# Kernel optimization log

Hardware: AMD Instinct MI355X
Metric: run time of the kernel (lower is better)

## Reference

```python
import jax, jax.numpy as jnp
import numpy as np

N, H, V = 2048, 2048, 32000

def setup_inputs() -> dict:
    key = jax.random.key(0)
    k1, k2, k3 = jax.random.split(key, 3)
    x = jax.random.normal(k1, (N, H), dtype=jnp.float32)
    y = jax.random.normal(k2, (N, V), dtype=jnp.float32)
    # nn.Linear default init: U(-1/sqrt(H), 1/sqrt(H))
    bound = 1.0 / np.sqrt(H)
    W = jax.random.uniform(k3, (V, H), dtype=jnp.float32, minval=-bound, maxval=bound)
    return {"x": x, "y": y, "W": W}

def reference(x, y, W):
    # logits = x @ W^T : [N, V]
    logits = jnp.einsum('nh,vh->nv', x, W)
    # MSE with 'mean' reduction over all elements
    diff = logits - y
    return jnp.mean(diff * diff)
```

## Files before the change

### kernel.cpp

```cpp
#include <hip/hip_runtime.h>

#define MDIM 2048
#define KDIM 2048
#define VDIM 32000
#define TILE 128
#define BK 64
#define LDAB (2 * KDIM)

typedef __bf16 bf16x8 __attribute__((ext_vector_type(8)));
typedef float f32x4 __attribute__((ext_vector_type(4)));
typedef unsigned short ushort_t;

__device__ __forceinline__ unsigned short f32_to_bf16_rne(float f) {
    unsigned u = __float_as_uint(f);
    u += 0x7FFFu + ((u >> 16) & 1u);
    return (unsigned short)(u >> 16);
}

__global__ __launch_bounds__(256) void cast_inplace_rows4_kernel(
        float* __restrict__ rows, float* zero_out) {
    if (zero_out && blockIdx.x == 0 && threadIdx.x == 0) *zero_out = 0.0f;
    float* base = rows + (long)blockIdx.x * 4 * KDIM;
    const int t = threadIdx.x;
    float4 v[8];
#pragma unroll
    for (int rr = 0; rr < 4; ++rr) {
        const float4* p = reinterpret_cast<const float4*>(base + rr * KDIM + t * 8);
        v[2 * rr]     = p[0];
        v[2 * rr + 1] = p[1];
    }
    __syncthreads();
#pragma unroll
    for (int rr = 0; rr < 4; ++rr) {
        union { unsigned short h[8]; uint4 u; } r;
        float4 a = v[2 * rr], b = v[2 * rr + 1];
        r.h[0] = f32_to_bf16_rne(a.x);
        r.h[1] = f32_to_bf16_rne(a.y);
        r.h[2] = f32_to_bf16_rne(a.z);
        r.h[3] = f32_to_bf16_rne(a.w);
        r.h[4] = f32_to_bf16_rne(b.x);
        r.h[5] = f32_to_bf16_rne(b.y);
        r.h[6] = f32_to_bf16_rne(b.z);
        r.h[7] = f32_to_bf16_rne(b.w);
        reinterpret_cast<uint4*>(base + rr * KDIM)[t] = r.u;
    }
}

__global__ __launch_bounds__(256) void gemm_mse_kernel(
        const unsigned short* __restrict__ A,
        const unsigned short* __restrict__ B,
        const float* __restrict__ Y,
        float* __restrict__ out) {
    __shared__ __align__(16) unsigned short As[TILE * BK];
    __shared__ __align__(16) unsigned short Bs[TILE * BK];

    const int tid  = threadIdx.x;
    const int lane = tid & 63;
    const int wave = tid >> 6;
    const int wr = (wave >> 1) * 64;
    const int wc = (wave & 1) * 64;
    const int m0 = lane & 15;
    const int q  = lane >> 4;

    const long rowBase = (long)blockIdx.x * TILE;
    const long colBase = (long)blockIdx.y * TILE;

    f32x4 acc[4][4];
#pragma unroll
    for (int i = 0; i < 4; ++i)
#pragma unroll
        for (int j = 0; j < 4; ++j)
            acc[i][j] = (f32x4){0.f, 0.f, 0.f, 0.f};

    const unsigned short* agp[4];
    const unsigned short* bgp[4];
    unsigned short* asp[4];
    unsigned short* bsp[4];
#pragma unroll
    for (int s = 0; s < 4; ++s) {
        int l = tid + 256 * s;
        int row = l >> 3;
        int segg = (l & 7) ^ (row & 7);
        agp[s] = A + (rowBase + row) * LDAB + segg * 8;
        bgp[s] = B + (colBase + row) * LDAB + segg * 8;
        asp[s] = As + l * 8;
        bsp[s] = Bs + l * 8;
    }

    const int sxor = m0 & 7;
    const unsigned short* aRow = As + (wr + m0) * BK;
    const unsigned short* bRow = Bs + (wc + m0) * BK;
    const int off0 = ((q)     ^ sxor) * 8;
    const int off1 = ((4 + q) ^ sxor) * 8;

    for (int kt = 0; kt < KDIM; kt += BK) {
        __syncthreads();
#pragma unroll
        for (int s = 0; s < 4; ++s) {
            __builtin_amdgcn_global_load_lds(
                (const __attribute__((address_space(1))) void*)(agp[s] + kt),
                (__attribute__((address_space(3))) void*)asp[s], 16, 0, 0);
            __builtin_amdgcn_global_load_lds(
                (const __attribute__((address_space(1))) void*)(bgp[s] + kt),
                (__attribute__((address_space(3))) void*)bsp[s], 16, 0, 0);
        }
        __syncthreads();

#pragma unroll
        for (int h = 0; h < 2; ++h) {
            const int off = h ? off1 : off0;
            bf16x8 af[4], bfr[4];
#pragma unroll
            for (int i = 0; i < 4; ++i)
                af[i] = *(const bf16x8*)(const void*)(aRow + i * 16 * BK + off);
#pragma unroll
            for (int j = 0; j < 4; ++j)
                bfr[j] = *(const bf16x8*)(const void*)(bRow + j * 16 * BK + off);
#pragma unroll
            for (int i = 0; i < 4; ++i)
#pragma unroll
                for (int j = 0; j < 4; ++j)
                    acc[i][j] = __builtin_amdgcn_mfma_f32_16x16x32_bf16(
                        af[i], bfr[j], acc[i][j], 0, 0, 0);
        }
    }

    float sum = 0.f;
#pragma unroll
    for (int i = 0; i < 4; ++i) {
#pragma unroll
        for (int j = 0; j < 4; ++j) {
            long gr = rowBase + wr + i * 16 + q * 4;
            long gc = colBase + wc + j * 16 + m0;
            const float* yp = Y + gr * VDIM + gc;
#pragma unroll
            for (int r = 0; r < 4; ++r) {
                float d = acc[i][j][r] - yp[(long)r * VDIM];
                sum += d * d;
            }
        }
    }
    sum += __shfl_down(sum, 32);
    sum += __shfl_down(sum, 16);
    sum += __shfl_down(sum, 8);
    sum += __shfl_down(sum, 4);
    sum += __shfl_down(sum, 2);
    sum += __shfl_down(sum, 1);
    __syncthreads();
    float* red = (float*)(void*)As;
    if (lane == 0) red[wave] = sum;
    __syncthreads();
    if (tid == 0) {
        float t = (red[0] + red[1]) + (red[2] + red[3]);
        atomicAdd(out, t * (1.0f / ((float)MDIM * (float)VDIM)));
    }
}

extern "C" void kernel_launch(void* const* d_in, const int* in_sizes, int n_in,
                              void* d_out, int out_size, void* d_ws, size_t ws_size,
                              hipStream_t stream) {
    float* x = (float*)d_in[0];
    const float* y = (const float*)d_in[1];
    float* W = (float*)d_in[2];
    float* out = (float*)d_out;
    (void)d_ws; (void)ws_size;

    cast_inplace_rows4_kernel<<<MDIM / 4, 256, 0, stream>>>(x, out);
    cast_inplace_rows4_kernel<<<VDIM / 4, 256, 0, stream>>>(W, nullptr);

    dim3 grid(MDIM / TILE, VDIM / TILE);
    gemm_mse_kernel<<<grid, 256, 0, stream>>>(
        (const unsigned short*)x, (const unsigned short*)W, y, out);
}
```

Before: 814.7 us.

## Use 256x256 tiles with double-buffered 8-phase pipelined MFMA GEMM and tile swizzle

Grows the block tile to 256x256 with 512 threads and 8 waves per block. The main loop becomes a hand-scheduled 8-phase pipeline over double-buffered LDS: asynchronous global-to-LDS loads for the next K slices are issued between MFMA groups, with explicit vmcnt and lgkmcnt waits, barriers and raised wave priority. It also remaps block indices with a swizzle so that consecutive blocks share W tiles in cache. The aim is to hide global load latency and raise arithmetic intensity, at the cost of more registers and LDS per block and a fragile manual wait-count schedule.

```diff
diff --git a/kernel.cpp b/kernel.cpp
--- a/kernel.cpp
+++ b/kernel.cpp
@@ -3,13 +3,13 @@
 #define MDIM 2048
 #define KDIM 2048
 #define VDIM 32000
-#define TILE 128
+#define BM 256
+#define BN 256
 #define BK 64
 #define LDAB (2 * KDIM)
 
 typedef __bf16 bf16x8 __attribute__((ext_vector_type(8)));
 typedef float f32x4 __attribute__((ext_vector_type(4)));
-typedef unsigned short ushort_t;
 
 __device__ __forceinline__ unsigned short f32_to_bf16_rne(float f) {
     unsigned u = __float_as_uint(f);
@@ -46,96 +46,159 @@
     }
 }
 
-__global__ __launch_bounds__(256) void gemm_mse_kernel(
+
+#define BMFMA(a, b, c) __builtin_amdgcn_mfma_f32_16x16x32_bf16(a, b, c, 0, 0, 0)
+
+#define GLL16(gp, lp) __builtin_amdgcn_global_load_lds( \
+    (const __attribute__((address_space(1))) void*)(gp), \
+    (__attribute__((address_space(3))) void*)(lp), 16, 0, 0)
+
+#define STAGE_A(bi, hf, kt) do { \
+    GLL16(aG0 + (size_t)(hf) * 128 * LDAB + (kt), &As[bi][(hf) * 128 * BK + dOff0]); \
+    GLL16(aG1 + (size_t)(hf) * 128 * LDAB + (kt), &As[bi][(hf) * 128 * BK + dOff1]); \
+} while (0)
+
+#define STAGE_B(bi, hf, kt) do { \
+    GLL16(bG0 + (size_t)(hf) * 128 * LDAB + (kt), &Bs[bi][(hf) * 128 * BK + dOff0]); \
+    GLL16(bG1 + (size_t)(hf) * 128 * LDAB + (kt), &Bs[bi][(hf) * 128 * BK + dOff1]); \
+} while (0)
+
+#define DS_B1(bi, n) do { \
+    const unsigned short* br_ = &Bs[bi][(wcol + (n) * 16 + m0) * BK]; \
+    bfr[2 * (n)]     = *(const bf16x8*)(const void*)(br_ + off0); \
+    bfr[2 * (n) + 1] = *(const bf16x8*)(const void*)(br_ + off1); \
+} while (0)
+#define DS_B8(bi) do { DS_B1(bi, 0); DS_B1(bi, 1); DS_B1(bi, 2); DS_B1(bi, 3); } while (0)
+
+#define DS_A2(bi, mb) do { \
+    const unsigned short* ar_ = &As[bi][(wrow + (mb) * 16 + m0) * BK]; \
+    af[0] = *(const bf16x8*)(const void*)(ar_ + off0); \
+    af[1] = *(const bf16x8*)(const void*)(ar_ + off1); \
+    af[2] = *(const bf16x8*)(const void*)(ar_ + 16 * BK + off0); \
+    af[3] = *(const bf16x8*)(const void*)(ar_ + 16 * BK + off1); \
+} while (0)
+
+#define MFMA16(mb) do { \
+    acc[(mb)][0]     = BMFMA(af[0], bfr[0], acc[(mb)][0]); \
+    acc[(mb) + 1][0] = BMFMA(af[2], bfr[0], acc[(mb) + 1][0]); \
+    acc[(mb)][1]     = BMFMA(af[0], bfr[2], acc[(mb)][1]); \
+    acc[(mb) + 1][1] = BMFMA(af[2], bfr[2], acc[(mb) + 1][1]); \
+    acc[(mb)][2]     = BMFMA(af[0], bfr[4], acc[(mb)][2]); \
+    acc[(mb) + 1][2] = BMFMA(af[2], bfr[4], acc[(mb) + 1][2]); \
+    acc[(mb)][3]     = BMFMA(af[0], bfr[6], acc[(mb)][3]); \
+    acc[(mb) + 1][3] = BMFMA(af[2], bfr[6], acc[(mb) + 1][3]); \
+    acc[(mb)][0]     = BMFMA(af[1], bfr[1], acc[(mb)][0]); \
+    acc[(mb) + 1][0] = BMFMA(af[3], bfr[1], acc[(mb) + 1][0]); \
+    acc[(mb)][1]     = BMFMA(af[1], bfr[3], acc[(mb)][1]); \
+    acc[(mb) + 1][1] = BMFMA(af[3], bfr[3], acc[(mb) + 1][1]); \
+    acc[(mb)][2]     = BMFMA(af[1], bfr[5], acc[(mb)][2]); \
+    acc[(mb) + 1][2] = BMFMA(af[3], bfr[5], acc[(mb) + 1][2]); \
+    acc[(mb)][3]     = BMFMA(af[1], bfr[7], acc[(mb)][3]); \
+    acc[(mb) + 1][3] = BMFMA(af[3], bfr[7], acc[(mb) + 1][3]); \
+} while (0)
+
+#define BAR() do { __builtin_amdgcn_s_barrier(); __builtin_amdgcn_sched_barrier(0); } while (0)
+#define WAITKL() do { asm volatile("s_waitcnt lgkmcnt(0)" ::: "memory"); \
+                      __builtin_amdgcn_sched_barrier(0); } while (0)
+#define VMCNT4() do { asm volatile("s_waitcnt vmcnt(4)" ::: "memory"); \
+                      __builtin_amdgcn_sched_barrier(0); } while (0)
+#define VMCNT0() do { asm volatile("s_waitcnt vmcnt(0)" ::: "memory"); \
+                      __builtin_amdgcn_sched_barrier(0); } while (0)
+
+#define PHASE(dsr, stg, wt, bi, mb) do { \
+    dsr; stg; wt; \
+    BAR(); WAITKL(); \
+    __builtin_amdgcn_s_setprio(1); \
+    MFMA16(mb); \
+    __builtin_amdgcn_s_setprio(0); \
+    BAR(); \
+} while (0)
+
+__global__ __launch_bounds__(512, 2) void gemm_mse_kernel(
         const unsigned short* __restrict__ A,
         const unsigned short* __restrict__ B,
         const float* __restrict__ Y,
         float* __restrict__ out) {
-    __shared__ __align__(16) unsigned short As[TILE * BK];
-    __shared__ __align__(16) unsigned short Bs[TILE * BK];
+    __shared__ __align__(16) unsigned short As[2][BM * BK];
+    __shared__ __align__(16) unsigned short Bs[2][BN * BK];
 
     const int tid  = threadIdx.x;
     const int lane = tid & 63;
-    const int wave = tid >> 6;
-    const int wr = (wave >> 1) * 64;
-    const int wc = (wave & 1) * 64;
+    const int wid  = tid >> 6;
+    const int wrow = (wid >> 2) * 128;
+    const int wcol = (wid & 3) * 64;
     const int m0 = lane & 15;
     const int q  = lane >> 4;
 
-    const long rowBase = (long)blockIdx.x * TILE;
-    const long colBase = (long)blockIdx.y * TILE;
-
-    f32x4 acc[4][4];
-#pragma unroll
-    for (int i = 0; i < 4; ++i)
+    const int lin = blockIdx.x;
+    const int swz = (lin & 7) * 125 + (lin >> 3);
+    const int tm = swz & 7;
+    const int tv = swz >> 3;
+    const long rowBase = (long)tm * BM;
+    const long colBase = (long)tv * BN;
+
+    f32x4 acc[8][4];
+#pragma unroll
+    for (int i = 0; i < 8; ++i)
 #pragma unroll
         for (int j = 0; j < 4; ++j)
             acc[i][j] = (f32x4){0.f, 0.f, 0.f, 0.f};
 
-    const unsigned short* agp[4];
-    const unsigned short* bgp[4];
-    unsigned short* asp[4];
-    unsigned short* bsp[4];
-#pragma unroll
-    for (int s = 0; s < 4; ++s) {
-        int l = tid + 256 * s;
-        int row = l >> 3;
-        int segg = (l & 7) ^ (row & 7);
-        agp[s] = A + (rowBase + row) * LDAB + segg * 8;
-        bgp[s] = B + (colBase + row) * LDAB + segg * 8;
-        asp[s] = As + l * 8;
-        bsp[s] = Bs + l * 8;
-    }
+    const int l0 = tid, l1 = tid + 512;
+    const int r0 = l0 >> 3, r1 = l1 >> 3;
+    const int g0 = (l0 & 7) ^ (r0 & 7), g1 = (l1 & 7) ^ (r1 & 7);
+    const unsigned short* aG0 = A + (size_t)(rowBase + r0) * LDAB + g0 * 8;
+    const unsigned short* aG1 = A + (size_t)(rowBase + r1) * LDAB + g1 * 8;
+    const unsigned short* bG0 = B + (size_t)(colBase + r0) * LDAB + g0 * 8;
+    const unsigned short* bG1 = B + (size_t)(colBase + r1) * LDAB + g1 * 8;
+    const int dOff0 = l0 * 8, dOff1 = l1 * 8;
 
     const int sxor = m0 & 7;
-    const unsigned short* aRow = As + (wr + m0) * BK;
-    const unsigned short* bRow = Bs + (wc + m0) * BK;
-    const int off0 = ((q)     ^ sxor) * 8;
+    const int off0 = ((0 + q) ^ sxor) * 8;
     const int off1 = ((4 + q) ^ sxor) * 8;
 
-    for (int kt = 0; kt < KDIM; kt += BK) {
-        __syncthreads();
-#pragma unroll
-        for (int s = 0; s < 4; ++s) {
-            __builtin_amdgcn_global_load_lds(
-                (const __attribute__((address_space(1))) void*)(agp[s] + kt),
-                (__attribute__((address_space(3))) void*)asp[s], 16, 0, 0);
-            __builtin_amdgcn_global_load_lds(
-                (const __attribute__((address_space(1))) void*)(bgp[s] + kt),
-                (__attribute__((address_space(3))) void*)bsp[s], 16, 0, 0);
-        }
-        __syncthreads();
-
-#pragma unroll
-        for (int h = 0; h < 2; ++h) {
-            const int off = h ? off1 : off0;
-            bf16x8 af[4], bfr[4];
-#pragma unroll
-            for (int i = 0; i < 4; ++i)
-                af[i] = *(const bf16x8*)(const void*)(aRow + i * 16 * BK + off);
-#pragma unroll
-            for (int j = 0; j < 4; ++j)
-                bfr[j] = *(const bf16x8*)(const void*)(bRow + j * 16 * BK + off);
-#pragma unroll
-            for (int i = 0; i < 4; ++i)
-#pragma unroll
-                for (int j = 0; j < 4; ++j)
-                    acc[i][j] = __builtin_amdgcn_mfma_f32_16x16x32_bf16(
-                        af[i], bfr[j], acc[i][j], 0, 0, 0);
-        }
-    }
+    bf16x8 af[4];
+    bf16x8 bfr[8];
+
+    STAGE_A(0, 0, 0); STAGE_A(0, 1, 0);
+    STAGE_B(0, 0, 0); STAGE_B(0, 1, 0);
+    STAGE_B(1, 0, BK); STAGE_B(1, 1, BK);
+    VMCNT4();
+    BAR();
+
+    for (int i = 0; i < 16; ++i) {
+        const int ktb  = i * 2 * BK;
+        const int ktA1 = ktb + BK;
+        int ktN  = ktb + 2 * BK;
+        if (ktN  > KDIM - BK) ktN  = KDIM - BK;
+        int ktN1 = ktb + 3 * BK;
+        if (ktN1 > KDIM - BK) ktN1 = KDIM - BK;
+
+        PHASE({ DS_B8(0); DS_A2(0, 0); },
+              { STAGE_A(1, 0, ktA1); STAGE_A(1, 1, ktA1); }, , 0, 0);
+        PHASE(DS_A2(0, 2), STAGE_B(0, 0, ktN), , 0, 2);
+        PHASE(DS_A2(0, 4), STAGE_B(0, 1, ktN), , 0, 4);
+        PHASE(DS_A2(0, 6), , VMCNT4(), 0, 6);
+        PHASE({ DS_B8(1); DS_A2(1, 0); }, STAGE_A(0, 0, ktN), , 1, 0);
+        PHASE(DS_A2(1, 2), STAGE_A(0, 1, ktN), , 1, 2);
+        PHASE(DS_A2(1, 4), STAGE_B(1, 0, ktN1), , 1, 4);
+        PHASE(DS_A2(1, 6), STAGE_B(1, 1, ktN1), VMCNT4(), 1, 6);
+    }
+
+    VMCNT0();
+    BAR();
 
     float sum = 0.f;
 #pragma unroll
-    for (int i = 0; i < 4; ++i) {
-#pragma unroll
-        for (int j = 0; j < 4; ++j) {
-            long gr = rowBase + wr + i * 16 + q * 4;
-            long gc = colBase + wc + j * 16 + m0;
-            const float* yp = Y + gr * VDIM + gc;
+    for (int m = 0; m < 8; ++m) {
+#pragma unroll
+        for (int n = 0; n < 4; ++n) {
+            long gr = rowBase + wrow + m * 16 + q * 4;
+            long gc = colBase + wcol + n * 16 + m0;
+            const float* yp = Y + gr * (long)VDIM + gc;
 #pragma unroll
             for (int r = 0; r < 4; ++r) {
-                float d = acc[i][j][r] - yp[(long)r * VDIM];
+                float d = acc[m][n][r] - yp[(long)r * VDIM];
                 sum += d * d;
             }
         }
@@ -146,12 +209,13 @@
     sum += __shfl_down(sum, 4);
     sum += __shfl_down(sum, 2);
     sum += __shfl_down(sum, 1);
-    __syncthreads();
     float* red = (float*)(void*)As;
-    if (lane == 0) red[wave] = sum;
+    if (lane == 0) red[wid] = sum;
     __syncthreads();
     if (tid == 0) {
-        float t = (red[0] + red[1]) + (red[2] + red[3]);
+        float t = 0.f;
+#pragma unroll
+        for (int w = 0; w < 8; ++w) t += red[w];
         atomicAdd(out, t * (1.0f / ((float)MDIM * (float)VDIM)));
     }
 }
@@ -168,7 +232,7 @@
     cast_inplace_rows4_kernel<<<MDIM / 4, 256, 0, stream>>>(x, out);
     cast_inplace_rows4_kernel<<<VDIM / 4, 256, 0, stream>>>(W, nullptr);
 
-    dim3 grid(MDIM / TILE, VDIM / TILE);
-    gemm_mse_kernel<<<grid, 256, 0, stream>>>(
+    dim3 grid((MDIM / BM) * (VDIM / BN));
+    gemm_mse_kernel<<<grid, 512, 0, stream>>>(
         (const unsigned short*)x, (const unsigned short*)W, y, out);
 }
```

New measurement: 740.2 us. 9.1% less time.

## Use 256x256 tiles with double-buffered LDS, 32x32 MFMA, and swizzled grid

Applied to the files above, without the earlier changes.

The GEMM+MSE kernel moves from 128x128 tiles to 256x256 tiles with 32x32x16 bf16 MFMA. It double-buffers LDS so global-to-LDS loads for the next K tile overlap compute, and it interleaves LDS fragment reads with MFMA groups using explicit waitcnt and setprio. A 1D grid with swizzled tile ordering is meant to improve L2 reuse, and Y is now read with float4 loads. The bigger tile raises arithmetic intensity but uses 128 KB of LDS and many registers, which forces one block per CU. The grid shrinks to 1000 blocks over 256 CUs, leaving some tail imbalance.

```diff
diff --git a/kernel.cpp b/kernel.cpp
--- a/kernel.cpp
+++ b/kernel.cpp
@@ -3,13 +3,14 @@
 #define MDIM 2048
 #define KDIM 2048
 #define VDIM 32000
-#define TILE 128
+#define BM 256
+#define BN 256
 #define BK 64
+#define NT (KDIM / BK)
 #define LDAB (2 * KDIM)
 
 typedef __bf16 bf16x8 __attribute__((ext_vector_type(8)));
-typedef float f32x4 __attribute__((ext_vector_type(4)));
-typedef unsigned short ushort_t;
+typedef float f32x16 __attribute__((ext_vector_type(16)));
 
 __device__ __forceinline__ unsigned short f32_to_bf16_rne(float f) {
     unsigned u = __float_as_uint(f);
@@ -46,97 +47,150 @@
     }
 }
 
-__global__ __launch_bounds__(256) void gemm_mse_kernel(
+
+#define MFMA3216(a, b, c) __builtin_amdgcn_mfma_f32_32x32x16_bf16(a, b, c, 0, 0, 0)
+
+#define GLL16(gp, lp) __builtin_amdgcn_global_load_lds( \
+    (const __attribute__((address_space(1))) void*)(gp), \
+    (__attribute__((address_space(3))) void*)(lp), 16, 0, 0)
+
+#define STAGE(bi, kt) do { \
+    _Pragma("unroll") \
+    for (int s_ = 0; s_ < 8; ++s_) { \
+        GLL16(aG + (size_t)32 * s_ * LDAB + (kt), &As[(bi)][tid8 + 2048 * s_]); \
+        GLL16(bG + (size_t)32 * s_ * LDAB + (kt), &Bs[(bi)][tid8 + 2048 * s_]); \
+    } \
+} while (0)
+
+#define SGO(ks) ((((2 * (ks)) + kh) ^ xorv) * 8)
+
+#define RDF(bi, ks, AF, BF) do { \
+    const unsigned short* aB_ = &As[(bi)][rowA * BK]; \
+    const unsigned short* bB_ = &Bs[(bi)][rowB * BK]; \
+    AF[0] = *(const bf16x8*)(const void*)(aB_ + SGO(ks)); \
+    AF[1] = *(const bf16x8*)(const void*)(aB_ + 32 * BK + SGO(ks)); \
+    AF[2] = *(const bf16x8*)(const void*)(aB_ + 64 * BK + SGO(ks)); \
+    AF[3] = *(const bf16x8*)(const void*)(aB_ + 96 * BK + SGO(ks)); \
+    BF[0] = *(const bf16x8*)(const void*)(bB_ + SGO(ks)); \
+    BF[1] = *(const bf16x8*)(const void*)(bB_ + 32 * BK + SGO(ks)); \
+    BF[2] = *(const bf16x8*)(const void*)(bB_ + 64 * BK + SGO(ks)); \
+    BF[3] = *(const bf16x8*)(const void*)(bB_ + 96 * BK + SGO(ks)); \
+} while (0)
+
+#define MM16(AF, BF) do { \
+    acc[0][0] = MFMA3216(BF[0], AF[0], acc[0][0]); \
+    acc[0][1] = MFMA3216(BF[1], AF[0], acc[0][1]); \
+    acc[0][2] = MFMA3216(BF[2], AF[0], acc[0][2]); \
+    acc[0][3] = MFMA3216(BF[3], AF[0], acc[0][3]); \
+    acc[1][0] = MFMA3216(BF[0], AF[1], acc[1][0]); \
+    acc[1][1] = MFMA3216(BF[1], AF[1], acc[1][1]); \
+    acc[1][2] = MFMA3216(BF[2], AF[1], acc[1][2]); \
+    acc[1][3] = MFMA3216(BF[3], AF[1], acc[1][3]); \
+    acc[2][0] = MFMA3216(BF[0], AF[2], acc[2][0]); \
+    acc[2][1] = MFMA3216(BF[1], AF[2], acc[2][1]); \
+    acc[2][2] = MFMA3216(BF[2], AF[2], acc[2][2]); \
+    acc[2][3] = MFMA3216(BF[3], AF[2], acc[2][3]); \
+    acc[3][0] = MFMA3216(BF[0], AF[3], acc[3][0]); \
+    acc[3][1] = MFMA3216(BF[1], AF[3], acc[3][1]); \
+    acc[3][2] = MFMA3216(BF[2], AF[3], acc[3][2]); \
+    acc[3][3] = MFMA3216(BF[3], AF[3], acc[3][3]); \
+} while (0)
+
+#define SCHEDB() __builtin_amdgcn_sched_barrier(0)
+#define LGKM(n)  do { asm volatile("s_waitcnt lgkmcnt(" #n ")" ::: "memory"); SCHEDB(); } while (0)
+#define VM0()    do { asm volatile("s_waitcnt vmcnt(0)" ::: "memory"); SCHEDB(); } while (0)
+
+#define KTILE(bi, ktN) do { \
+    RDF(bi, 0, af0, bf0); \
+    STAGE((bi) ^ 1, ktN); \
+    RDF(bi, 1, af1, bf1); \
+    LGKM(8); \
+    __builtin_amdgcn_s_setprio(1); MM16(af0, bf0); __builtin_amdgcn_s_setprio(0); \
+    RDF(bi, 2, af0, bf0); \
+    LGKM(8); \
+    __builtin_amdgcn_s_setprio(1); MM16(af1, bf1); __builtin_amdgcn_s_setprio(0); \
+    RDF(bi, 3, af1, bf1); \
+    LGKM(8); \
+    __builtin_amdgcn_s_setprio(1); MM16(af0, bf0); __builtin_amdgcn_s_setprio(0); \
+    LGKM(0); \
+    __builtin_amdgcn_s_setprio(1); MM16(af1, bf1); __builtin_amdgcn_s_setprio(0); \
+    VM0(); \
+    __builtin_amdgcn_s_barrier(); SCHEDB(); \
+} while (0)
+
+__global__ __launch_bounds__(256, 1) void gemm_mse_kernel(
         const unsigned short* __restrict__ A,
         const unsigned short* __restrict__ B,
         const float* __restrict__ Y,
         float* __restrict__ out) {
-    __shared__ __align__(16) unsigned short As[TILE * BK];
-    __shared__ __align__(16) unsigned short Bs[TILE * BK];
+    __shared__ __align__(16) unsigned short As[2][BM * BK];
+    __shared__ __align__(16) unsigned short Bs[2][BN * BK];
 
     const int tid  = threadIdx.x;
     const int lane = tid & 63;
-    const int wave = tid >> 6;
-    const int wr = (wave >> 1) * 64;
-    const int wc = (wave & 1) * 64;
-    const int m0 = lane & 15;
-    const int q  = lane >> 4;
-
-    const long rowBase = (long)blockIdx.x * TILE;
-    const long colBase = (long)blockIdx.y * TILE;
-
-    f32x4 acc[4][4];
-#pragma unroll
-    for (int i = 0; i < 4; ++i)
-#pragma unroll
-        for (int j = 0; j < 4; ++j)
-            acc[i][j] = (f32x4){0.f, 0.f, 0.f, 0.f};
-
-    const unsigned short* agp[4];
-    const unsigned short* bgp[4];
-    unsigned short* asp[4];
-    unsigned short* bsp[4];
-#pragma unroll
-    for (int s = 0; s < 4; ++s) {
-        int l = tid + 256 * s;
-        int row = l >> 3;
-        int segg = (l & 7) ^ (row & 7);
-        agp[s] = A + (rowBase + row) * LDAB + segg * 8;
-        bgp[s] = B + (colBase + row) * LDAB + segg * 8;
-        asp[s] = As + l * 8;
-        bsp[s] = Bs + l * 8;
-    }
-
-    const int sxor = m0 & 7;
-    const unsigned short* aRow = As + (wr + m0) * BK;
-    const unsigned short* bRow = Bs + (wc + m0) * BK;
-    const int off0 = ((q)     ^ sxor) * 8;
-    const int off1 = ((4 + q) ^ sxor) * 8;
-
-    for (int kt = 0; kt < KDIM; kt += BK) {
-        __syncthreads();
-#pragma unroll
-        for (int s = 0; s < 4; ++s) {
-            __builtin_amdgcn_global_load_lds(
-                (const __attribute__((address_space(1))) void*)(agp[s] + kt),
-                (__attribute__((address_space(3))) void*)asp[s], 16, 0, 0);
-            __builtin_amdgcn_global_load_lds(
-                (const __attribute__((address_space(1))) void*)(bgp[s] + kt),
-                (__attribute__((address_space(3))) void*)bsp[s], 16, 0, 0);
-        }
-        __syncthreads();
-
-#pragma unroll
-        for (int h = 0; h < 2; ++h) {
-            const int off = h ? off1 : off0;
-            bf16x8 af[4], bfr[4];
-#pragma unroll
-            for (int i = 0; i < 4; ++i)
-                af[i] = *(const bf16x8*)(const void*)(aRow + i * 16 * BK + off);
-#pragma unroll
-            for (int j = 0; j < 4; ++j)
-                bfr[j] = *(const bf16x8*)(const void*)(bRow + j * 16 * BK + off);
-#pragma unroll
-            for (int i = 0; i < 4; ++i)
-#pragma unroll
-                for (int j = 0; j < 4; ++j)
-                    acc[i][j] = __builtin_amdgcn_mfma_f32_16x16x32_bf16(
-                        af[i], bfr[j], acc[i][j], 0, 0, 0);
-        }
+    const int wid  = tid >> 6;
+    const int wrow = (wid >> 1) * 128;
+    const int wcol = (wid & 1) * 128;
+    const int l31  = lane & 31;
+    const int kh   = lane >> 5;
+    const int xorv = lane & 7;
+
+    const int lin = blockIdx.x;
+    const int swz = (lin & 7) * 125 + (lin >> 3);
+    const int tm = swz & 7;
+    const int tv = swz >> 3;
+    const long rowBase = (long)tm * BM;
+    const long colBase = (long)tv * BN;
+
+    f32x16 acc[4][4];
+    {
+        const f32x16 z = {0.f,0.f,0.f,0.f,0.f,0.f,0.f,0.f,
+                          0.f,0.f,0.f,0.f,0.f,0.f,0.f,0.f};
+#pragma unroll
+        for (int m = 0; m < 4; ++m)
+#pragma unroll
+            for (int n = 0; n < 4; ++n)
+                acc[m][n] = z;
+    }
+
+    const int srow = tid >> 3;
+    const int g0   = (tid & 7) ^ (srow & 7);
+    const unsigned short* aG = A + (size_t)(rowBase + srow) * LDAB + g0 * 8;
+    const unsigned short* bG = B + (size_t)(colBase + srow) * LDAB + g0 * 8;
+    const int tid8 = tid * 8;
+
+    const int rowA = wrow + l31;
+    const int rowB = wcol + l31;
+
+    bf16x8 af0[4], bf0[4], af1[4], bf1[4];
+
+    STAGE(0, 0);
+    VM0();
+    __builtin_amdgcn_s_barrier(); SCHEDB();
+
+    for (int tt = 0; tt < 16; ++tt) {
+        const int ktn0 = (2 * tt + 1) * BK;
+        int ktn1 = (2 * tt + 2) * BK;
+        if (ktn1 > KDIM - BK) ktn1 = KDIM - BK;
+        KTILE(0, ktn0);
+        KTILE(1, ktn1);
     }
 
     float sum = 0.f;
 #pragma unroll
-    for (int i = 0; i < 4; ++i) {
-#pragma unroll
-        for (int j = 0; j < 4; ++j) {
-            long gr = rowBase + wr + i * 16 + q * 4;
-            long gc = colBase + wc + j * 16 + m0;
-            const float* yp = Y + gr * VDIM + gc;
-#pragma unroll
-            for (int r = 0; r < 4; ++r) {
-                float d = acc[i][j][r] - yp[(long)r * VDIM];
-                sum += d * d;
+    for (int m = 0; m < 4; ++m) {
+        const long gr = rowBase + wrow + m * 32 + l31;
+        const float* yr = Y + gr * (long)VDIM + colBase + wcol + 4 * kh;
+#pragma unroll
+        for (int n = 0; n < 4; ++n) {
+#pragma unroll
+            for (int Q = 0; Q < 4; ++Q) {
+                float4 yv = *(const float4*)(yr + n * 32 + 8 * Q);
+                float d0 = acc[m][n][4 * Q + 0] - yv.x;
+                float d1 = acc[m][n][4 * Q + 1] - yv.y;
+                float d2 = acc[m][n][4 * Q + 2] - yv.z;
+                float d3 = acc[m][n][4 * Q + 3] - yv.w;
+                sum += d0 * d0 + d1 * d1 + d2 * d2 + d3 * d3;
             }
         }
     }
@@ -146,9 +200,8 @@
     sum += __shfl_down(sum, 4);
     sum += __shfl_down(sum, 2);
     sum += __shfl_down(sum, 1);
-    __syncthreads();
     float* red = (float*)(void*)As;
-    if (lane == 0) red[wave] = sum;
+    if (lane == 0) red[wid] = sum;
     __syncthreads();
     if (tid == 0) {
         float t = (red[0] + red[1]) + (red[2] + red[3]);
@@ -168,7 +221,7 @@
     cast_inplace_rows4_kernel<<<MDIM / 4, 256, 0, stream>>>(x, out);
     cast_inplace_rows4_kernel<<<VDIM / 4, 256, 0, stream>>>(W, nullptr);
 
-    dim3 grid(MDIM / TILE, VDIM / TILE);
+    dim3 grid((MDIM / BM) * (VDIM / BN));
     gemm_mse_kernel<<<grid, 256, 0, stream>>>(
         (const unsigned short*)x, (const unsigned short*)W, y, out);
 }
```

Result: slower. 857.0 us (+5.2%).
